# Kernel optimization log

Hardware: AMD Instinct MI355X
Metric: run time of the kernel (lower is better)

## Reference

```python
import jax, jax.numpy as jnp
import numpy as np

BS, N, N_HEAD, F_IN, F_OUT = 8, 1024, 8, 256, 64
NEG_SLOPE = 0.2


def setup_inputs() -> dict:
    key = jax.random.key(0)
    k_h, k_adj, k_w, k_src, k_dst = jax.random.split(key, 5)
    h = jax.random.normal(k_h, (BS, N, F_IN), dtype=jnp.float32)
    adj = jax.random.randint(k_adj, (BS, N, N), 0, 2) > 0  # bool adjacency
    # xavier_uniform-style params
    def xavier(k, shape, fan_in, fan_out):
        limit = float(np.sqrt(6.0 / (fan_in + fan_out)))
        return jax.random.uniform(k, shape, jnp.float32, -limit, limit)
    w = xavier(k_w, (N_HEAD, F_IN, F_OUT), F_IN, F_OUT)
    a_src = xavier(k_src, (N_HEAD, F_OUT, 1), F_OUT, 1)
    a_dst = xavier(k_dst, (N_HEAD, F_OUT, 1), F_OUT, 1)
    bias = jnp.zeros((F_OUT,), dtype=jnp.float32)
    return {"h": h, "adj": adj, "w": w, "a_src": a_src, "a_dst": a_dst, "bias": bias}


def reference(h, adj, w, a_src, a_dst, bias):
    # h: [bs, n, f_in], w: [n_head, f_in, f_out]
    h_prime = jnp.einsum('bnf,hfo->bhno', h, w)            # [bs, h, n, f_out]
    t = jnp.tanh(h_prime)
    attn_src = jnp.einsum('bhno,ho->bhn', t, a_src[..., 0])  # [bs, h, n]
    attn_dst = jnp.einsum('bhno,ho->bhn', t, a_dst[..., 0])  # [bs, h, n]
    attn = attn_src[:, :, :, None] + attn_dst[:, :, None, :]  # [bs, h, n, n]
    attn = jnp.where(attn >= 0, attn, NEG_SLOPE * attn)       # leaky_relu(0.2)
    n = adj.shape[-1]
    mask = ~(adj[:, None, :, :] | jnp.eye(n, dtype=bool))     # [bs, 1->h, n, n]
    attn = jnp.where(mask, -jnp.inf, attn)
    attn = jax.nn.softmax(attn, axis=-1)                      # diag always valid
    out = jnp.einsum('bhnm,bhmo->bhno', attn, h_prime)
    return out + bias
```

## Files before the change

### kernel.cpp

```cpp
#include <hip/hip_runtime.h>
#include <math.h>

#define BS 8
#define NPTS 1024
#define NH 8
#define FIN 256
#define FOUT 64

typedef __attribute__((ext_vector_type(8))) short s8v;
typedef __attribute__((ext_vector_type(8))) _Float16 h8v;
typedef __attribute__((ext_vector_type(2))) __fp16 fp16x2;
typedef __attribute__((ext_vector_type(4))) float f4v;
typedef unsigned long long u64;

__device__ __forceinline__ unsigned short f2bf(float f) {
  unsigned u = __float_as_uint(f);
  return (unsigned short)((u + 0x7fffu + ((u >> 16) & 1u)) >> 16);
}
__device__ __forceinline__ float bf2f(unsigned short s) {
  return __uint_as_float(((unsigned)s) << 16);
}
__device__ __forceinline__ float fast_tanh(float x) {
  float e = __expf(2.f * x);
  return 1.f - 2.f / (e + 1.f);
}
__device__ __forceinline__ float hw_exp2(float x) {
  float r;
  asm("v_exp_f32 %0, %1" : "=v"(r) : "v"(x));
  return r;
}

__device__ __forceinline__ void gl_lds16(const void* g, void* l) {
  __builtin_amdgcn_global_load_lds(
      (const __attribute__((address_space(1))) unsigned*)g,
      (__attribute__((address_space(3))) unsigned*)l, 16, 0, 0);
}

__global__ __launch_bounds__(256) void prep_kernel(
    const void* __restrict__ adjv, const float* __restrict__ w,
    const float* __restrict__ h,
    u64* __restrict__ abits,
    unsigned short* __restrict__ wT_hi, unsigned short* __restrict__ wT_lo,
    unsigned short* __restrict__ hs_hi, unsigned short* __restrict__ hs_lo)
{
  const int blk = blockIdx.x;
  const int t = threadIdx.x;
  if (blk < 2048) {
    __shared__ int badsh;
    if (t == 0) badsh = 0;
    __syncthreads();
    if (((const unsigned*)adjv)[t] > 1u) badsh = 1;
    __syncthreads();
    const int lane = t & 63;
    const int gw = blk * 4 + (t >> 6);
    const int b = gw >> 10, i = gw & 1023;
    const int m16 = lane & 15, g = lane >> 4;
    u64 words[4];
    if (badsh == 0) {
      const int4* row4 = (const int4*)((const int*)adjv + ((size_t)b * NPTS + i) * NPTS);
      int4 av[4];
      av[0] = row4[lane]; av[1] = row4[lane + 64];
      av[2] = row4[lane + 128]; av[3] = row4[lane + 192];
#pragma unroll
      for (int ci = 0; ci < 4; ++ci) {
        unsigned n = (unsigned)(av[ci].x != 0) | ((unsigned)(av[ci].y != 0) << 1) |
                     ((unsigned)(av[ci].z != 0) << 2) | ((unsigned)(av[ci].w != 0) << 3);
        unsigned d = (unsigned)(i - (ci * 256 + 4 * lane));
        if (d < 4u) n |= 1u << d;
        u64 val = (u64)n << (4 * m16);
#pragma unroll
        for (int msk = 1; msk <= 8; msk <<= 1)
          val |= (u64)__shfl_xor(val, msk, 64);
        words[ci] = val;
      }
    } else {
      const unsigned* rowB = (const unsigned*)((const unsigned char*)adjv + ((size_t)b * NPTS + i) * NPTS);
      unsigned av[4];
      av[0] = rowB[lane]; av[1] = rowB[lane + 64];
      av[2] = rowB[lane + 128]; av[3] = rowB[lane + 192];
#pragma unroll
      for (int ci = 0; ci < 4; ++ci) {
        unsigned v = av[ci];
        unsigned n = ((v & 0xffu) ? 1u : 0u) | (((v >> 8) & 0xffu) ? 2u : 0u) |
                     (((v >> 16) & 0xffu) ? 4u : 0u) | ((v >> 24) ? 8u : 0u);
        unsigned d = (unsigned)(i - (ci * 256 + 4 * lane));
        if (d < 4u) n |= 1u << d;
        u64 val = (u64)n << (4 * m16);
#pragma unroll
        for (int msk = 1; msk <= 8; msk <<= 1)
          val |= (u64)__shfl_xor(val, msk, 64);
        words[ci] = val;
      }
    }
    if (m16 == 0) {
#pragma unroll
      for (int ci = 0; ci < 4; ++ci)
        abits[((size_t)b * NPTS + i) * 16 + ci * 4 + g] = words[ci];
    }
  } else if (blk < 2112) {
    const int bb = blk - 2048;
    const int hh = bb >> 3, ks = bb & 7;
    const int o = t & 63, kq = t >> 6;
#pragma unroll
    for (int e = 0; e < 8; ++e) {
      int k = ks * 32 + kq * 8 + e;
      float v = w[((size_t)hh * FIN + k) * FOUT + o];
      unsigned short hi = f2bf(v);
      wT_hi[((size_t)hh * FOUT + o) * FIN + k] = hi;
      wT_lo[((size_t)hh * FOUT + o) * FIN + k] = f2bf(v - bf2f(hi));
    }
  } else {
    const size_t g = (size_t)(blk - 2112) * 256 + t;
    const float4* hp4 = (const float4*)h + g * 2;
    float4 v0 = hp4[0], v1 = hp4[1];
    float vv[8] = {v0.x, v0.y, v0.z, v0.w, v1.x, v1.y, v1.z, v1.w};
    unsigned short hb[8], lb[8];
#pragma unroll
    for (int e = 0; e < 8; ++e) {
      unsigned u = __float_as_uint(vv[e]);
      float r = vv[e] - __uint_as_float(u & 0xffff0000u);
      hb[e] = (unsigned short)(u >> 16);
      lb[e] = (unsigned short)(__float_as_uint(r) >> 16);
    }
    *(uint4*)(hs_hi + g * 8) = *(const uint4*)&hb[0];
    *(uint4*)(hs_lo + g * 8) = *(const uint4*)&lb[0];
  }
}

__global__ __launch_bounds__(256, 4) void proj_kernel(
    const unsigned short* __restrict__ hs_hi, const unsigned short* __restrict__ hs_lo,
    const unsigned short* __restrict__ wT_hi, const unsigned short* __restrict__ wT_lo,
    const float* __restrict__ a_src, const float* __restrict__ a_dst,
    unsigned short* __restrict__ hfrag,
    float* __restrict__ srcb, float* __restrict__ dstb)
{
  __shared__ unsigned short Bbuf[2][4096];
  __shared__ float tile[64][65];

  const int t = threadIdx.x;
  const int lane = t & 63;
  const int wv = t >> 6;
  const int blk = blockIdx.x;
  const int hh = blk & 7;
  const int q  = blk >> 3;
  const int b  = q >> 4;
  const int it = q & 15;
  const int i0 = it * 64;
  const int bh = b * NH + hh;
  const int l15 = lane & 15;
  const int g4  = lane >> 4;
  const int koff = g4 * 8;

  const int o_t  = t >> 2;
  const int gsrc = (t & 3) ^ ((o_t >> 1) & 3);
  const unsigned short* gB_hi = wT_hi + ((size_t)(hh * FOUT + o_t)) * FIN + gsrc * 8;
  const unsigned short* gB_lo = wT_lo + ((size_t)(hh * FOUT + o_t)) * FIN + gsrc * 8;

  const unsigned short* arow_hi = hs_hi + ((size_t)(b * NPTS + i0 + wv * 16 + l15)) * FIN + koff;
  const unsigned short* arow_lo = hs_lo + ((size_t)(b * NPTS + i0 + wv * 16 + l15)) * FIN + koff;

  const int sw = (l15 >> 1) & 3;
  int roff[4];
#pragma unroll
  for (int nt = 0; nt < 4; ++nt)
    roff[nt] = (nt * 16 + l15) * 32 + (g4 ^ sw) * 8;

  gl_lds16(gB_hi, &Bbuf[0][wv * 512]);
  gl_lds16(gB_lo, &Bbuf[0][2048 + wv * 512]);
  s8v Ah = *(const s8v*)(arow_hi);
  s8v Al = *(const s8v*)(arow_lo);

  f4v acc[4];
#pragma unroll
  for (int nt = 0; nt < 4; ++nt) acc[nt] = 0.0f;
  __syncthreads();

#pragma unroll
  for (int k0 = 0; k0 < 8; ++k0) {
    const int buf = k0 & 1;
    s8v Ah_n = Ah, Al_n = Al;
    if (k0 < 7) {
      gl_lds16(gB_hi + (k0 + 1) * 32, &Bbuf[buf ^ 1][wv * 512]);
      gl_lds16(gB_lo + (k0 + 1) * 32, &Bbuf[buf ^ 1][2048 + wv * 512]);
      Ah_n = *(const s8v*)(arow_hi + (k0 + 1) * 32);
      Al_n = *(const s8v*)(arow_lo + (k0 + 1) * 32);
    }
    const unsigned short* fb = &Bbuf[buf][0];
#pragma unroll
    for (int nt = 0; nt < 4; ++nt) {
      s8v Bh = *(const s8v*)(fb + roff[nt]);
      s8v Bl = *(const s8v*)(fb + 2048 + roff[nt]);
      acc[nt] = __builtin_amdgcn_mfma_f32_16x16x32_bf16(Ah, Bh, acc[nt], 0, 0, 0);
      acc[nt] = __builtin_amdgcn_mfma_f32_16x16x32_bf16(Al, Bh, acc[nt], 0, 0, 0);
      acc[nt] = __builtin_amdgcn_mfma_f32_16x16x32_bf16(Ah, Bl, acc[nt], 0, 0, 0);
    }
    Ah = Ah_n; Al = Al_n;
    __syncthreads();
  }

  float a_s[4], a_d[4];
#pragma unroll
  for (int nt = 0; nt < 4; ++nt) {
    a_s[nt] = a_src[hh * FOUT + nt * 16 + l15];
    a_d[nt] = a_dst[hh * FOUT + nt * 16 + l15];
  }
#pragma unroll
  for (int qq = 0; qq < 4; ++qq) {
    float ps = 0.f, pd = 0.f;
#pragma unroll
    for (int nt = 0; nt < 4; ++nt) {
      float tv = fast_tanh(acc[nt][qq]);
      ps = fmaf(tv, a_s[nt], ps);
      pd = fmaf(tv, a_d[nt], pd);
    }
#pragma unroll
    for (int m = 8; m >= 1; m >>= 1) {
      ps += __shfl_xor(ps, m, 64);
      pd += __shfl_xor(pd, m, 64);
    }
    if (l15 == 0) {
      int row = i0 + wv * 16 + g4 * 4 + qq;
      srcb[(size_t)bh * NPTS + row] = ps;
      dstb[(size_t)bh * NPTS + row] = pd;
    }
  }

#pragma unroll
  for (int nt = 0; nt < 4; ++nt)
#pragma unroll
    for (int qq = 0; qq < 4; ++qq)
      tile[wv * 16 + g4 * 4 + qq][nt * 16 + l15] = acc[nt][qq];
  __syncthreads();

  const int cbase = t >> 6;
#pragma unroll
  for (int ci = 0; ci < 2; ++ci) {
    int cc = cbase + ci * 4;
    int ks = cc >> 2, nt2 = cc & 3;
    int jb = ks * 32 + ((lane >> 4) * 8);
    int ob = nt2 * 16 + l15;
    h8v v;
#pragma unroll
    for (int e = 0; e < 8; ++e) v[e] = (_Float16)tile[jb + e][ob];
    *(h8v*)(hfrag + (((size_t)(bh * 16 + it) * 8 + cc) * 64 + lane) * 8) = v;
  }
}

__global__ __launch_bounds__(256, 4) void attn_kernel(
    const u64* __restrict__ abits,
    const unsigned short* __restrict__ hfrag,
    const float* __restrict__ srcb, const float* __restrict__ dstb,
    const float* __restrict__ bias, float* __restrict__ out)
{
  __shared__ float dsh[NPTS];
  __shared__ float wred[4];
  __shared__ unsigned short frag[2][4096];

  const int t = threadIdx.x;
  const int lane = t & 63;
  const int wv = t >> 6;
  const int blk = blockIdx.x;
  const int hh = blk & 7;
  const int q  = blk >> 3;
  const int b  = q >> 4;
  const int it = q & 15;
  const int i0 = it * 64;
  const int bh = b * NH + hh;
  const int l15 = lane & 15;
  const int koff = (lane >> 4) * 8;
  const int rowA = i0 + wv * 16 + l15;

  const uint4* fgb = (const uint4*)hfrag + (size_t)bh * 16 * 512;
  const u64* abrow = abits + ((size_t)b * NPTS + rowA) * 16;

  uint4 s0 = fgb[t];
  uint4 s1 = fgb[t + 256];
  u64 ab_cur = abrow[0];
  const float src_r = srcb[(size_t)bh * NPTS + rowA];
  float4 dv = ((const float4*)(dstb + (size_t)bh * NPTS))[t];

  const float L2E = 1.44269504f;
  float4 dsc;
  dsc.x = dv.x * L2E; dsc.y = dv.y * L2E; dsc.z = dv.z * L2E; dsc.w = dv.w * L2E;
  ((float4*)dsh)[t] = dsc;
  float lm = fmaxf(fmaxf(dv.x, dv.y), fmaxf(dv.z, dv.w));
#pragma unroll
  for (int m = 32; m >= 1; m >>= 1) lm = fmaxf(lm, __shfl_xor(lm, m, 64));
  if (lane == 0) wred[wv] = lm;
  __syncthreads();
  const float M = fmaxf(fmaxf(wred[0], wred[1]), fmaxf(wred[2], wred[3]));
  const float xm = src_r + M;
  const float m_row = fmaxf(xm, 0.2f * xm);
  const float c1s = (src_r - m_row) * L2E;
  const float c2s = (0.2f * src_r - m_row) * L2E;

  ((uint4*)&frag[0][0])[t]       = s0;
  ((uint4*)&frag[0][0])[t + 256] = s1;
  __syncthreads();

  float l = 0.f;
  f4v acc[4];
#pragma unroll
  for (int nt = 0; nt < 4; ++nt) acc[nt] = 0.0f;

#pragma unroll 2
  for (int jt = 0; jt < 16; ++jt) {
    const int buf = jt & 1;
    uint4 n0, n1; u64 ab_nxt;
    if (jt < 15) {
      const uint4* fgn = fgb + (size_t)(jt + 1) * 512;
      n0 = fgn[t];
      n1 = fgn[t + 256];
      ab_nxt = abrow[jt + 1];
    }
    __builtin_amdgcn_sched_barrier(0);

    const int jb = jt * 64 + koff;
    float4 d0 = *(const float4*)&dsh[jb];
    float4 d1 = *(const float4*)&dsh[jb + 4];
    float4 d2 = *(const float4*)&dsh[jb + 32];
    float4 d3 = *(const float4*)&dsh[jb + 36];
    float dl0[8] = {d0.x, d0.y, d0.z, d0.w, d1.x, d1.y, d1.z, d1.w};
    float dl1[8] = {d2.x, d2.y, d2.z, d2.w, d3.x, d3.y, d3.z, d3.w};
    const unsigned w0 = (unsigned)(ab_cur) >> koff;
    const unsigned w1 = (unsigned)(ab_cur >> 32) >> koff;
    float pe0[8], pe1[8];
#pragma unroll
    for (int e = 0; e < 8; ++e) {
      float arg = fmaxf(c1s + dl0[e], fmaf(0.2f, dl0[e], c2s));
      arg = ((w0 >> e) & 1u) ? arg : -__builtin_inff();
      float pe = hw_exp2(arg);
      l += pe;
      pe0[e] = pe;
    }
#pragma unroll
    for (int e = 0; e < 8; ++e) {
      float arg = fmaxf(c1s + dl1[e], fmaf(0.2f, dl1[e], c2s));
      arg = ((w1 >> e) & 1u) ? arg : -__builtin_inff();
      float pe = hw_exp2(arg);
      l += pe;
      pe1[e] = pe;
    }
    union { fp16x2 q[4]; h8v v; } ua, ub;
    ua.q[0] = __builtin_amdgcn_cvt_pkrtz(pe0[0], pe0[1]);
    ua.q[1] = __builtin_amdgcn_cvt_pkrtz(pe0[2], pe0[3]);
    ua.q[2] = __builtin_amdgcn_cvt_pkrtz(pe0[4], pe0[5]);
    ua.q[3] = __builtin_amdgcn_cvt_pkrtz(pe0[6], pe0[7]);
    ub.q[0] = __builtin_amdgcn_cvt_pkrtz(pe1[0], pe1[1]);
    ub.q[1] = __builtin_amdgcn_cvt_pkrtz(pe1[2], pe1[3]);
    ub.q[2] = __builtin_amdgcn_cvt_pkrtz(pe1[4], pe1[5]);
    ub.q[3] = __builtin_amdgcn_cvt_pkrtz(pe1[6], pe1[7]);
    h8v pa0 = ua.v;
    h8v pa1 = ub.v;

    __builtin_amdgcn_s_setprio(1);
#pragma unroll
    for (int nt = 0; nt < 4; ++nt) {
      h8v B0 = *(const h8v*)&frag[buf][(nt * 64 + lane) * 8];
      acc[nt] = __builtin_amdgcn_mfma_f32_16x16x32_f16(pa0, B0, acc[nt], 0, 0, 0);
    }
#pragma unroll
    for (int nt = 0; nt < 4; ++nt) {
      h8v B1 = *(const h8v*)&frag[buf][((4 + nt) * 64 + lane) * 8];
      acc[nt] = __builtin_amdgcn_mfma_f32_16x16x32_f16(pa1, B1, acc[nt], 0, 0, 0);
    }
    __builtin_amdgcn_s_setprio(0);

    if (jt < 15) {
      ((uint4*)&frag[buf ^ 1][0])[t]       = n0;
      ((uint4*)&frag[buf ^ 1][0])[t + 256] = n1;
      ab_cur = ab_nxt;
    }
    __syncthreads();
  }

  l += __shfl_xor(l, 16, 64);
  l += __shfl_xor(l, 32, 64);

  float bias4[4];
#pragma unroll
  for (int nt = 0; nt < 4; ++nt) bias4[nt] = bias[nt * 16 + l15];

#pragma unroll
  for (int qq = 0; qq < 4; ++qq) {
    float lq = __shfl(l, (lane >> 4) * 4 + qq, 64);
    float linv = 1.0f / lq;
    int rowq = i0 + wv * 16 + (lane >> 4) * 4 + qq;
    size_t ob = ((size_t)bh * NPTS + rowq) * FOUT;
#pragma unroll
    for (int nt = 0; nt < 4; ++nt)
      out[ob + nt * 16 + l15] = acc[nt][qq] * linv + bias4[nt];
  }
}

extern "C" void kernel_launch(void* const* d_in, const int* in_sizes, int n_in,
                              void* d_out, int out_size, void* d_ws, size_t ws_size,
                              hipStream_t stream)
{
  const float* h     = (const float*)d_in[0];
  const void*  adj   = d_in[1];
  const float* w     = (const float*)d_in[2];
  const float* a_src = (const float*)d_in[3];
  const float* a_dst = (const float*)d_in[4];
  const float* bias  = (const float*)d_in[5];
  float* out = (float*)d_out;

  char* p = (char*)d_ws;
  float* srcb = (float*)p;                      p += (size_t)BS * NH * NPTS * 4;
  float* dstb = (float*)p;                      p += (size_t)BS * NH * NPTS * 4;
  unsigned short* wT_hi = (unsigned short*)p;   p += (size_t)NH * FOUT * FIN * 2;
  unsigned short* wT_lo = (unsigned short*)p;   p += (size_t)NH * FOUT * FIN * 2;
  u64* abits = (u64*)p;                         p += (size_t)BS * NPTS * 16 * 8;
  unsigned short* hs_hi = (unsigned short*)p;   p += (size_t)BS * NPTS * FIN * 2;
  unsigned short* hs_lo = (unsigned short*)p;   p += (size_t)BS * NPTS * FIN * 2;
  unsigned short* hfrag = (unsigned short*)p;

  prep_kernel<<<dim3(3136), dim3(256), 0, stream>>>(
      adj, w, h, abits, wT_hi, wT_lo, hs_hi, hs_lo);
  proj_kernel<<<dim3(1024), dim3(256), 0, stream>>>(
      hs_hi, hs_lo, wT_hi, wT_lo, a_src, a_dst, hfrag, srcb, dstb);
  attn_kernel<<<dim3(1024), dim3(256), 0, stream>>>(
      abits, hfrag, srcb, dstb, bias, out);
}
```

Before: 57.80 us.

## Compute softmax denominator via MFMA ones-column and mask probabilities with LUT

Removes the per-element mask select and the scalar row-sum accumulation. The adjacency mask is now applied as a bitwise AND on the packed fp16 probabilities using a small shared-memory lookup table. The row sum comes from an extra MFMA against an all-ones operand, which also sums the fp16-rounded values and so matches the numerator. Block index decoding is also reordered so that consecutive blocks walk row tiles within one head, which changes L2 locality. The cost is two extra MFMAs per iteration plus four LDS lookups.

```diff
diff --git a/kernel.cpp b/kernel.cpp
--- a/kernel.cpp
+++ b/kernel.cpp
@@ -141,10 +141,9 @@
   const int lane = t & 63;
   const int wv = t >> 6;
   const int blk = blockIdx.x;
-  const int hh = blk & 7;
-  const int q  = blk >> 3;
-  const int b  = q >> 4;
-  const int it = q & 15;
+  const int it = blk & 15;
+  const int hh = (blk >> 4) & 7;
+  const int b  = blk >> 7;
   const int i0 = it * 64;
   const int bh = b * NH + hh;
   const int l15 = lane & 15;
@@ -254,16 +253,16 @@
 {
   __shared__ float dsh[NPTS];
   __shared__ float wred[4];
+  __shared__ uint2 mlut[16];
   __shared__ unsigned short frag[2][4096];
 
   const int t = threadIdx.x;
   const int lane = t & 63;
   const int wv = t >> 6;
   const int blk = blockIdx.x;
-  const int hh = blk & 7;
-  const int q  = blk >> 3;
-  const int b  = q >> 4;
-  const int it = q & 15;
+  const int it = blk & 15;
+  const int hh = (blk >> 4) & 7;
+  const int b  = blk >> 7;
   const int i0 = it * 64;
   const int bh = b * NH + hh;
   const int l15 = lane & 15;
@@ -278,6 +277,13 @@
   u64 ab_cur = abrow[0];
   const float src_r = srcb[(size_t)bh * NPTS + rowA];
   float4 dv = ((const float4*)(dstb + (size_t)bh * NPTS))[t];
+
+  if (t < 16) {
+    unsigned m = t;
+    mlut[t] = make_uint2(
+        ((m & 1u) ? 0xFFFFu : 0u) | (((m >> 1) & 1u) ? 0xFFFF0000u : 0u),
+        (((m >> 2) & 1u) ? 0xFFFFu : 0u) | (((m >> 3) & 1u) ? 0xFFFF0000u : 0u));
+  }
 
   const float L2E = 1.44269504f;
   float4 dsc;
@@ -298,10 +304,14 @@
   ((uint4*)&frag[0][0])[t + 256] = s1;
   __syncthreads();
 
-  float l = 0.f;
-  f4v acc[4];
+  h8v ones;
+#pragma unroll
+  for (int e = 0; e < 8; ++e) ones[e] = (_Float16)1.0f;
+
+  f4v acc[4], acc_l;
 #pragma unroll
   for (int nt = 0; nt < 4; ++nt) acc[nt] = 0.0f;
+  acc_l = 0.0f;
 
 #pragma unroll 2
   for (int jt = 0; jt < 16; ++jt) {
@@ -328,20 +338,14 @@
 #pragma unroll
     for (int e = 0; e < 8; ++e) {
       float arg = fmaxf(c1s + dl0[e], fmaf(0.2f, dl0[e], c2s));
-      arg = ((w0 >> e) & 1u) ? arg : -__builtin_inff();
-      float pe = hw_exp2(arg);
-      l += pe;
-      pe0[e] = pe;
+      pe0[e] = hw_exp2(arg);
     }
 #pragma unroll
     for (int e = 0; e < 8; ++e) {
       float arg = fmaxf(c1s + dl1[e], fmaf(0.2f, dl1[e], c2s));
-      arg = ((w1 >> e) & 1u) ? arg : -__builtin_inff();
-      float pe = hw_exp2(arg);
-      l += pe;
-      pe1[e] = pe;
-    }
-    union { fp16x2 q[4]; h8v v; } ua, ub;
+      pe1[e] = hw_exp2(arg);
+    }
+    union { fp16x2 q[4]; unsigned u[4]; h8v v; } ua, ub;
     ua.q[0] = __builtin_amdgcn_cvt_pkrtz(pe0[0], pe0[1]);
     ua.q[1] = __builtin_amdgcn_cvt_pkrtz(pe0[2], pe0[3]);
     ua.q[2] = __builtin_amdgcn_cvt_pkrtz(pe0[4], pe0[5]);
@@ -350,6 +354,12 @@
     ub.q[1] = __builtin_amdgcn_cvt_pkrtz(pe1[2], pe1[3]);
     ub.q[2] = __builtin_amdgcn_cvt_pkrtz(pe1[4], pe1[5]);
     ub.q[3] = __builtin_amdgcn_cvt_pkrtz(pe1[6], pe1[7]);
+    {
+      uint2 ma0 = mlut[w0 & 15], ma1 = mlut[(w0 >> 4) & 15];
+      uint2 mb0 = mlut[w1 & 15], mb1 = mlut[(w1 >> 4) & 15];
+      ua.u[0] &= ma0.x; ua.u[1] &= ma0.y; ua.u[2] &= ma1.x; ua.u[3] &= ma1.y;
+      ub.u[0] &= mb0.x; ub.u[1] &= mb0.y; ub.u[2] &= mb1.x; ub.u[3] &= mb1.y;
+    }
     h8v pa0 = ua.v;
     h8v pa1 = ub.v;
 
@@ -359,11 +369,13 @@
       h8v B0 = *(const h8v*)&frag[buf][(nt * 64 + lane) * 8];
       acc[nt] = __builtin_amdgcn_mfma_f32_16x16x32_f16(pa0, B0, acc[nt], 0, 0, 0);
     }
+    acc_l = __builtin_amdgcn_mfma_f32_16x16x32_f16(pa0, ones, acc_l, 0, 0, 0);
 #pragma unroll
     for (int nt = 0; nt < 4; ++nt) {
       h8v B1 = *(const h8v*)&frag[buf][((4 + nt) * 64 + lane) * 8];
       acc[nt] = __builtin_amdgcn_mfma_f32_16x16x32_f16(pa1, B1, acc[nt], 0, 0, 0);
     }
+    acc_l = __builtin_amdgcn_mfma_f32_16x16x32_f16(pa1, ones, acc_l, 0, 0, 0);
     __builtin_amdgcn_s_setprio(0);
 
     if (jt < 15) {
@@ -374,17 +386,13 @@
     __syncthreads();
   }
 
-  l += __shfl_xor(l, 16, 64);
-  l += __shfl_xor(l, 32, 64);
-
   float bias4[4];
 #pragma unroll
   for (int nt = 0; nt < 4; ++nt) bias4[nt] = bias[nt * 16 + l15];
 
 #pragma unroll
   for (int qq = 0; qq < 4; ++qq) {
-    float lq = __shfl(l, (lane >> 4) * 4 + qq, 64);
-    float linv = 1.0f / lq;
+    float linv = 1.0f / acc_l[qq];
     int rowq = i0 + wv * 16 + (lane >> 4) * 4 + qq;
     size_t ob = ((size_t)bh * NPTS + rowq) * FOUT;
 #pragma unroll
```

Measured after the change: 52.07 us. 9.9% less time.
